# Performance work log

Hardware: AMD Instinct MI355X
Metric: run time of the kernel (lower is better)

The kernel has to match this reference:

```python
import jax, jax.numpy as jnp
import numpy as np

D, H, W = 20, 18, 18      # f_dim = (20, 72//4, 72//4); depth == feature_ch
PI = 3.14159              # constant used in the torch module


def make_grid():
    # matches make_coordinate_grid_3d: normalized coords in [-1, 1]
    x = 2.0 * jnp.arange(W, dtype=jnp.float32) / (W - 1) - 1.0
    y = 2.0 * jnp.arange(H, dtype=jnp.float32) / (H - 1) - 1.0
    z = 2.0 * jnp.arange(D, dtype=jnp.float32) / (D - 1) - 1.0
    xx = jnp.broadcast_to(x[None, None, :], (D, H, W))
    yy = jnp.broadcast_to(y[None, :, None], (D, H, W))
    zz = jnp.broadcast_to(z[:, None, None], (D, H, W))
    grid_xy = jnp.stack([xx, yy], axis=-1)   # (D,H,W,2), order (x, y)
    return grid_xy, zz


def trilinear_sample(vol, grid):
    # vol: (D,H,W); grid: (D,H,W,3) with (x,y,z) in [-1,1]
    # F.grid_sample defaults: mode='bilinear' (trilinear), padding='zeros', align_corners=False
    ix = ((grid[..., 0] + 1.0) * W - 1.0) * 0.5
    iy = ((grid[..., 1] + 1.0) * H - 1.0) * 0.5
    iz = ((grid[..., 2] + 1.0) * D - 1.0) * 0.5
    x0, y0, z0 = jnp.floor(ix), jnp.floor(iy), jnp.floor(iz)
    wx, wy, wz = ix - x0, iy - y0, iz - z0
    vflat = vol.reshape(-1)
    out = jnp.zeros_like(ix)
    for cz in (0, 1):
        for cy in (0, 1):
            for cx in (0, 1):
                xi = x0 + cx
                yi = y0 + cy
                zi = z0 + cz
                w = ((wx if cx else 1.0 - wx)
                     * (wy if cy else 1.0 - wy)
                     * (wz if cz else 1.0 - wz))
                valid = ((xi >= 0) & (xi < W) & (yi >= 0) & (yi < H)
                         & (zi >= 0) & (zi < D))
                xi_c = jnp.clip(xi, 0, W - 1).astype(jnp.int32)
                yi_c = jnp.clip(yi, 0, H - 1).astype(jnp.int32)
                zi_c = jnp.clip(zi, 0, D - 1).astype(jnp.int32)
                idx = (zi_c * H + yi_c) * W + xi_c
                out = out + jnp.where(valid, w * vflat[idx], 0.0)
    return out


def setup_inputs() -> dict:
    key = jax.random.key(0)
    ks = jax.random.split(key, 10)
    B, P, F = 4096, 256, 20
    s = 0.05
    return {
        "feature_map": jax.random.normal(ks[0], (B, F, H, W), jnp.float32),
        "para_code": jax.random.normal(ks[1], (B, P), jnp.float32),
        "W1": jax.random.normal(ks[2], (P, P), jnp.float32) * s,
        "b1": jax.random.normal(ks[3], (P,), jnp.float32) * s,
        "Ws": jax.random.normal(ks[4], (P, F), jnp.float32) * s,
        "bs": jax.random.normal(ks[5], (F,), jnp.float32) * s,
        "Wr": jax.random.normal(ks[6], (P, F), jnp.float32) * s,
        "br": jax.random.normal(ks[7], (F,), jnp.float32) * s,
        "Wt": jax.random.normal(ks[8], (P, 2 * F), jnp.float32) * s,
        "bt": jax.random.normal(ks[9], (2 * F,), jnp.float32) * s,
    }


def reference(feature_map, para_code, W1, b1, Ws, bs, Wr, br, Wt, bt):
    B, F = feature_map.shape[0], feature_map.shape[1]  # F == D == 20
    grid_xy, grid_z = make_grid()
    h = jax.nn.relu(para_code @ W1 + b1)                     # commn_linear
    scale = jax.nn.sigmoid(h @ Ws + bs) * 2.0                # (B,F)
    angle = jnp.tanh(h @ Wr + br) * PI                       # (B,F)
    trans = jnp.tanh(h @ Wt + bt).reshape(B, F, 2)           # (B,F,2)
    c, s = jnp.cos(angle), jnp.sin(angle)
    rot = jnp.stack([jnp.stack([c, -s], -1),
                     jnp.stack([s, c], -1)], -2)             # (B,F,2,2)
    g = grid_xy.reshape(F, H * W, 2)                          # depth == feature_ch
    # per-channel affine: rotate, scale, translate each grid point
    tg = jnp.einsum('bfij,fpj->bfpi', rot, g)                 # (B,F,HW,2)
    tg = tg * scale[:, :, None, None] + trans[:, :, None, :]
    full_grid = jnp.concatenate(
        [tg.reshape(B, F, H, W, 2),
         jnp.broadcast_to(grid_z, (B, F, H, W))[..., None]], axis=-1)
    return jax.vmap(trilinear_sample)(feature_map, full_grid)
```

## Files before the change

kernel.cpp:

```cpp
#include <hip/hip_runtime.h>

#define PI_F 3.14159f

__global__ __launch_bounds__(256) void params_kernel(
    const float* __restrict__ pc, const float* __restrict__ W1, const float* __restrict__ b1,
    const float* __restrict__ Ws, const float* __restrict__ bs,
    const float* __restrict__ Wr, const float* __restrict__ br,
    const float* __restrict__ Wt, const float* __restrict__ bt,
    float* __restrict__ params)
{
    __shared__ float para[8][256];
    __shared__ float hbuf[8][260];
    __shared__ float raw[8][80];

    const int t  = threadIdx.x;
    const int b0 = blockIdx.x * 8;

    #pragma unroll
    for (int g = 0; g < 8; ++g) para[g][t] = pc[(size_t)(b0 + g) * 256 + t];
    __syncthreads();

    float acc[8];
    #pragma unroll
    for (int g = 0; g < 8; ++g) acc[g] = b1[t];
    for (int k = 0; k < 256; ++k) {
        float w = W1[k * 256 + t];
        #pragma unroll
        for (int g = 0; g < 8; ++g) acc[g] = fmaf(para[g][k], w, acc[g]);
    }
    #pragma unroll
    for (int g = 0; g < 8; ++g) hbuf[g][t] = fmaxf(acc[g], 0.0f);
    __syncthreads();

    for (int task = t; task < 640; task += 256) {
        int g   = task / 80;
        int col = task - g * 80;
        const float* Wcol;
        float bias;
        int stride;
        if (col < 20)      { Wcol = Ws + col;        bias = bs[col];      stride = 20; }
        else if (col < 40) { Wcol = Wr + (col - 20); bias = br[col - 20]; stride = 20; }
        else               { Wcol = Wt + (col - 40); bias = bt[col - 40]; stride = 40; }
        float a = bias;
        for (int k = 0; k < 256; ++k) a = fmaf(hbuf[g][k], Wcol[k * stride], a);
        raw[g][col] = a;
    }
    __syncthreads();

    for (int task = t; task < 160; task += 256) {
        int g = task / 20;
        int f = task - g * 20;
        float sc  = 2.0f / (1.0f + expf(-raw[g][f]));
        float ang = PI_F * tanhf(raw[g][20 + f]);
        float tx  = tanhf(raw[g][40 + 2 * f]);
        float ty  = tanhf(raw[g][40 + 2 * f + 1]);
        float c = cosf(ang), s = sinf(ang);
        float* o = params + ((size_t)(b0 + g) * 20 + f) * 8;
        o[0] = 9.0f * sc * c;  o[1] = -9.0f * sc * s;  o[2] = fmaf(9.0f, tx, 9.5f);
        o[3] = 9.0f * sc * s;  o[4] =  9.0f * sc * c;  o[5] = fmaf(9.0f, ty, 9.5f);
        o[6] = 0.0f;           o[7] = 0.0f;
    }
}

template<int D>
__device__ __forceinline__ void slice(const float* __restrict__ pb,
                                      const float* vol,
                                      float X, float Y,
                                      float* __restrict__ ob)
{
    constexpr int   Z0  = (D == 0) ? -1 : (40 * D - 19) / 38;
    constexpr float W1v = ((40.0f * D - 19.0f) - 38.0f * (float)Z0) / 38.0f;
    constexpr float W0v = 1.0f - W1v;
    constexpr bool  V0  = (Z0 >= 0);
    constexpr bool  V1  = (Z0 + 1 <= 19);

    float4 pA = *(const float4*)(pb + D * 8);
    float2 pB = *(const float2*)(pb + D * 8 + 4);

    float ix = fmaf(pA.x, X, fmaf(pA.y, Y, pA.z));
    float iy = fmaf(pA.w, X, fmaf(pB.x, Y, pB.y));

    float fx = floorf(ix), fy = floorf(iy);
    float u1 = ix - fx, v1 = iy - fy;
    float u0 = 1.0f - u1, v0 = 1.0f - v1;

    int x0 = (int)fx, y0 = (int)fy;
    int xc0 = min(max(x0, 0), 19), xc1 = min(max(x0 + 1, 0), 19);
    int yc0 = min(max(y0, 0), 19), yc1 = min(max(y0 + 1, 0), 19);

    int a00 = yc0 * 20 + xc0, a01 = yc0 * 20 + xc1;
    int a10 = yc1 * 20 + xc0, a11 = yc1 * 20 + xc1;

    float r0 = 0.0f, r1 = 0.0f;
    if constexpr (V0) {
        const float* s = vol + Z0 * 400;
        float t00 = s[a00], t01 = s[a01], t10 = s[a10], t11 = s[a11];
        r0 = fmaf(fmaf(t01, u1, t00 * u0), v0, fmaf(t11, u1, t10 * u0) * v1);
    }
    if constexpr (V1) {
        const float* s = vol + (Z0 + 1) * 400;
        float t00 = s[a00], t01 = s[a01], t10 = s[a10], t11 = s[a11];
        r1 = fmaf(fmaf(t01, u1, t00 * u0), v0, fmaf(t11, u1, t10 * u0) * v1);
    }

    float r;
    if constexpr (!V0)      r = r1 * W1v;
    else if constexpr (!V1) r = r0 * W0v;
    else                    r = fmaf(r0, W0v, r1 * W1v);

    ob[D * 324] = r;
}

template<int D>
struct Run {
    static __device__ __forceinline__ void go(const float* __restrict__ pb,
                                              const float* vol,
                                              float X, float Y,
                                              float* __restrict__ ob) {
        slice<D>(pb, vol, X, Y, ob);
        Run<D + 1>::go(pb, vol, X, Y, ob);
    }
};
template<>
struct Run<20> {
    static __device__ __forceinline__ void go(const float*, const float*,
                                              float, float, float*) {}
};

__global__ __launch_bounds__(384) void sample_kernel(
    const float* __restrict__ fmap, const float* __restrict__ params,
    float* __restrict__ out)
{
    __shared__ __align__(16) float vol[8000];

    const int b = blockIdx.x;
    const int t = threadIdx.x;

    float4* v4 = (float4*)vol;
    for (int i = t; i < 2000; i += 384) v4[i] = make_float4(0.f, 0.f, 0.f, 0.f);
    __syncthreads();

    const float* fb = fmap + (size_t)b * 6480;
    int yy = 0, xx = 0;
    if (t < 324) {
        yy = t / 18;
        xx = t - yy * 18;
        const int w = (yy + 1) * 20 + (xx + 1);
        #pragma unroll
        for (int dz = 0; dz < 20; ++dz)
            vol[dz * 400 + w] = fb[dz * 324 + t];
    }
    __syncthreads();

    if (t >= 324) return;

    const float X = xx * (2.0f / 17.0f) - 1.0f;
    const float Y = yy * (2.0f / 17.0f) - 1.0f;
    const float* pb = params + (size_t)b * 160;
    float* ob = out + (size_t)b * 6480 + t;

    Run<0>::go(pb, vol, X, Y, ob);
}

extern "C" void kernel_launch(void* const* d_in, const int* in_sizes, int n_in,
                              void* d_out, int out_size, void* d_ws, size_t ws_size,
                              hipStream_t stream)
{
    const float* fmap = (const float*)d_in[0];
    const float* pc   = (const float*)d_in[1];
    const float* W1   = (const float*)d_in[2];
    const float* b1   = (const float*)d_in[3];
    const float* Ws   = (const float*)d_in[4];
    const float* bs   = (const float*)d_in[5];
    const float* Wr   = (const float*)d_in[6];
    const float* br   = (const float*)d_in[7];
    const float* Wt   = (const float*)d_in[8];
    const float* bt   = (const float*)d_in[9];
    float* out    = (float*)d_out;
    float* params = (float*)d_ws;

    const int B = in_sizes[0] / (20 * 18 * 18);

    params_kernel<<<B / 8, 256, 0, stream>>>(pc, W1, b1, Ws, bs, Wr, br, Wt, bt, params);
    sample_kernel<<<B, 384, 0, stream>>>(fmap, params, out);
}
```

Before: 262.0 us.

## Precompute z-interpolated slices into padded LDS volume and use readlane in params GEMM

The sampler now applies the constant z-interpolation once per voxel while loading the volume, storing 20 pre-blended slices in a 22x22-padded LDS layout. Each output then needs only 4 bilinear LDS reads with no clamping branches, instead of 8 reads plus separate z-blending. The params kernel drops its 8-batch LDS staging for 4 batches per block, broadcasting para_code values with readlane, and vectorises the hbuf reads. The translation offset and clamp bounds shift to fit the wider padding.

```diff
diff --git a/kernel.cpp b/kernel.cpp
--- a/kernel.cpp
+++ b/kernel.cpp
@@ -9,30 +9,41 @@
     const float* __restrict__ Wt, const float* __restrict__ bt,
     float* __restrict__ params)
 {
-    __shared__ float para[8][256];
-    __shared__ float hbuf[8][260];
-    __shared__ float raw[8][80];
+    __shared__ float hbuf[4][260];
+    __shared__ float raw[4][80];
 
-    const int t  = threadIdx.x;
-    const int b0 = blockIdx.x * 8;
+    const int t    = threadIdx.x;
+    const int lane = t & 63;
+    const int b0   = blockIdx.x * 4;
+
+    float pval[4][4];
+    #pragma unroll
+    for (int g = 0; g < 4; ++g)
+        #pragma unroll
+        for (int c = 0; c < 4; ++c)
+            pval[g][c] = pc[(size_t)(b0 + g) * 256 + c * 64 + lane];
+
+    float acc[4];
+    #pragma unroll
+    for (int g = 0; g < 4; ++g) acc[g] = b1[t];
 
     #pragma unroll
-    for (int g = 0; g < 8; ++g) para[g][t] = pc[(size_t)(b0 + g) * 256 + t];
+    for (int c = 0; c < 4; ++c) {
+        for (int kk = 0; kk < 64; ++kk) {
+            float w = W1[(c * 64 + kk) * 256 + t];
+            #pragma unroll
+            for (int g = 0; g < 4; ++g) {
+                float pk = __int_as_float(
+                    __builtin_amdgcn_readlane(__float_as_int(pval[g][c]), kk));
+                acc[g] = fmaf(pk, w, acc[g]);
+            }
+        }
+    }
+    #pragma unroll
+    for (int g = 0; g < 4; ++g) hbuf[g][t] = fmaxf(acc[g], 0.0f);
     __syncthreads();
 
-    float acc[8];
-    #pragma unroll
-    for (int g = 0; g < 8; ++g) acc[g] = b1[t];
-    for (int k = 0; k < 256; ++k) {
-        float w = W1[k * 256 + t];
-        #pragma unroll
-        for (int g = 0; g < 8; ++g) acc[g] = fmaf(para[g][k], w, acc[g]);
-    }
-    #pragma unroll
-    for (int g = 0; g < 8; ++g) hbuf[g][t] = fmaxf(acc[g], 0.0f);
-    __syncthreads();
-
-    for (int task = t; task < 640; task += 256) {
+    for (int task = t; task < 320; task += 256) {
         int g   = task / 80;
         int col = task - g * 80;
         const float* Wcol;
@@ -41,13 +52,21 @@
         if (col < 20)      { Wcol = Ws + col;        bias = bs[col];      stride = 20; }
         else if (col < 40) { Wcol = Wr + (col - 20); bias = br[col - 20]; stride = 20; }
         else               { Wcol = Wt + (col - 40); bias = bt[col - 40]; stride = 40; }
+        const float4* h4 = (const float4*)hbuf[g];
         float a = bias;
-        for (int k = 0; k < 256; ++k) a = fmaf(hbuf[g][k], Wcol[k * stride], a);
+        for (int k4 = 0; k4 < 64; ++k4) {
+            float4 h = h4[k4];
+            int k = k4 * 4;
+            a = fmaf(h.x, Wcol[k * stride], a);
+            a = fmaf(h.y, Wcol[(k + 1) * stride], a);
+            a = fmaf(h.z, Wcol[(k + 2) * stride], a);
+            a = fmaf(h.w, Wcol[(k + 3) * stride], a);
+        }
         raw[g][col] = a;
     }
     __syncthreads();
 
-    for (int task = t; task < 160; task += 256) {
+    for (int task = t; task < 80; task += 256) {
         int g = task / 20;
         int f = task - g * 20;
         float sc  = 2.0f / (1.0f + expf(-raw[g][f]));
@@ -56,60 +75,32 @@
         float ty  = tanhf(raw[g][40 + 2 * f + 1]);
         float c = cosf(ang), s = sinf(ang);
         float* o = params + ((size_t)(b0 + g) * 20 + f) * 8;
-        o[0] = 9.0f * sc * c;  o[1] = -9.0f * sc * s;  o[2] = fmaf(9.0f, tx, 9.5f);
-        o[3] = 9.0f * sc * s;  o[4] =  9.0f * sc * c;  o[5] = fmaf(9.0f, ty, 9.5f);
+        o[0] = 9.0f * sc * c;  o[1] = -9.0f * sc * s;  o[2] = fmaf(9.0f, tx, 10.5f);
+        o[3] = 9.0f * sc * s;  o[4] =  9.0f * sc * c;  o[5] = fmaf(9.0f, ty, 10.5f);
         o[6] = 0.0f;           o[7] = 0.0f;
     }
 }
 
 template<int D>
-__device__ __forceinline__ void slice(const float* __restrict__ pb,
-                                      const float* vol,
-                                      float X, float Y,
-                                      float* __restrict__ ob)
-{
-    constexpr int   Z0  = (D == 0) ? -1 : (40 * D - 19) / 38;
-    constexpr float W1v = ((40.0f * D - 19.0f) - 38.0f * (float)Z0) / 38.0f;
-    constexpr float W0v = 1.0f - W1v;
-    constexpr bool  V0  = (Z0 >= 0);
-    constexpr bool  V1  = (Z0 + 1 <= 19);
+struct Stage {
+    static constexpr int   Z0  = (D == 0) ? -1 : (40 * D - 19) / 38;
+    static constexpr float W1v = (float)((40.0 * D - 19.0) / 38.0 - (double)Z0);
+    static constexpr float W0v = 1.0f - W1v;
+    static constexpr bool  V0  = (Z0 >= 0);
+    static constexpr bool  V1  = (Z0 + 1 <= 19);
 
-    float4 pA = *(const float4*)(pb + D * 8);
-    float2 pB = *(const float2*)(pb + D * 8 + 4);
-
-    float ix = fmaf(pA.x, X, fmaf(pA.y, Y, pA.z));
-    float iy = fmaf(pA.w, X, fmaf(pB.x, Y, pB.y));
-
-    float fx = floorf(ix), fy = floorf(iy);
-    float u1 = ix - fx, v1 = iy - fy;
-    float u0 = 1.0f - u1, v0 = 1.0f - v1;
-
-    int x0 = (int)fx, y0 = (int)fy;
-    int xc0 = min(max(x0, 0), 19), xc1 = min(max(x0 + 1, 0), 19);
-    int yc0 = min(max(y0, 0), 19), yc1 = min(max(y0 + 1, 0), 19);
-
-    int a00 = yc0 * 20 + xc0, a01 = yc0 * 20 + xc1;
-    int a10 = yc1 * 20 + xc0, a11 = yc1 * 20 + xc1;
-
-    float r0 = 0.0f, r1 = 0.0f;
-    if constexpr (V0) {
-        const float* s = vol + Z0 * 400;
-        float t00 = s[a00], t01 = s[a01], t10 = s[a10], t11 = s[a11];
-        r0 = fmaf(fmaf(t01, u1, t00 * u0), v0, fmaf(t11, u1, t10 * u0) * v1);
+    static __device__ __forceinline__ void go(const float (&v)[20], float* vol, int w) {
+        float I;
+        if constexpr (V0 && V1)  I = fmaf(v[Z0], W0v, v[Z0 + 1] * W1v);
+        else if constexpr (V0)   I = v[Z0] * W0v;
+        else                     I = v[(Z0 + 1) < 0 ? 0 : (Z0 + 1)] * W1v;
+        vol[D * 484 + w] = I;
+        Stage<D + 1>::go(v, vol, w);
     }
-    if constexpr (V1) {
-        const float* s = vol + (Z0 + 1) * 400;
-        float t00 = s[a00], t01 = s[a01], t10 = s[a10], t11 = s[a11];
-        r1 = fmaf(fmaf(t01, u1, t00 * u0), v0, fmaf(t11, u1, t10 * u0) * v1);
-    }
-
-    float r;
-    if constexpr (!V0)      r = r1 * W1v;
-    else if constexpr (!V1) r = r0 * W0v;
-    else                    r = fmaf(r0, W0v, r1 * W1v);
-
-    ob[D * 324] = r;
-}
+};
+template<> struct Stage<20> {
+    static __device__ __forceinline__ void go(const float (&)[20], float*, int) {}
+};
 
 template<int D>
 struct Run {
@@ -117,12 +108,30 @@
                                               const float* vol,
                                               float X, float Y,
                                               float* __restrict__ ob) {
-        slice<D>(pb, vol, X, Y, ob);
+        float4 pA = *(const float4*)(pb + D * 8);
+        float2 pB = *(const float2*)(pb + D * 8 + 4);
+
+        float ix = fmaf(pA.x, X, fmaf(pA.y, Y, pA.z));
+        float iy = fmaf(pA.w, X, fmaf(pB.x, Y, pB.y));
+
+        float fx = floorf(ix), fy = floorf(iy);
+        float u1 = ix - fx, v1 = iy - fy;
+        float u0 = 1.0f - u1, v0 = 1.0f - v1;
+
+        int xb = min(max((int)fx, 0), 20);
+        int yb = min(max((int)fy, 0), 20);
+
+        const float* s = vol + D * 484 + yb * 22 + xb;
+        float t00 = s[0], t01 = s[1], t10 = s[22], t11 = s[23];
+
+        float r = fmaf(fmaf(t01, u1, t00 * u0), v0,
+                       fmaf(t11, u1, t10 * u0) * v1);
+        ob[D * 324] = r;
+
         Run<D + 1>::go(pb, vol, X, Y, ob);
     }
 };
-template<>
-struct Run<20> {
+template<> struct Run<20> {
     static __device__ __forceinline__ void go(const float*, const float*,
                                               float, float, float*) {}
 };
@@ -131,24 +140,25 @@
     const float* __restrict__ fmap, const float* __restrict__ params,
     float* __restrict__ out)
 {
-    __shared__ __align__(16) float vol[8000];
+    __shared__ __align__(16) float vol[20 * 484];
 
     const int b = blockIdx.x;
     const int t = threadIdx.x;
 
     float4* v4 = (float4*)vol;
-    for (int i = t; i < 2000; i += 384) v4[i] = make_float4(0.f, 0.f, 0.f, 0.f);
+    for (int i = t; i < 2420; i += 384) v4[i] = make_float4(0.f, 0.f, 0.f, 0.f);
     __syncthreads();
 
-    const float* fb = fmap + (size_t)b * 6480;
     int yy = 0, xx = 0;
     if (t < 324) {
         yy = t / 18;
         xx = t - yy * 18;
-        const int w = (yy + 1) * 20 + (xx + 1);
+        const float* fb = fmap + (size_t)b * 6480;
+        float v[20];
         #pragma unroll
-        for (int dz = 0; dz < 20; ++dz)
-            vol[dz * 400 + w] = fb[dz * 324 + t];
+        for (int dz = 0; dz < 20; ++dz) v[dz] = fb[dz * 324 + t];
+        const int w = (yy + 2) * 22 + (xx + 2);
+        Stage<0>::go(v, vol, w);
     }
     __syncthreads();
 
@@ -181,6 +191,6 @@
 
     const int B = in_sizes[0] / (20 * 18 * 18);
 
-    params_kernel<<<B / 8, 256, 0, stream>>>(pc, W1, b1, Ws, bs, Wr, br, Wt, bt, params);
+    params_kernel<<<B / 4, 256, 0, stream>>>(pc, W1, b1, Ws, bs, Wr, br, Wt, bt, params);
     sample_kernel<<<B, 384, 0, stream>>>(fmap, params, out);
 }
```

Result: faster. 243.4 us (-7.1%).
